# Optimization experiments

Hardware: AMD Instinct MI355X
Metric: run time of the kernel (lower is better)

Reference implementation:

```python
import jax, jax.numpy as jnp
import numpy as np

# ---- static config (matches init_kwargs) ----
D_MODEL = 2048
D_STATE = 64
D_CONV = 4
EXPAND = 2
HEADDIM = 64
NGROUPS = 1
CHUNK = 256
D_INNER = EXPAND * D_MODEL            # 4096
NHEADS = D_INNER // HEADDIM           # 64
CONV_DIM = D_INNER + 2 * NGROUPS * D_STATE   # 4224
D_IN_PROJ = 2 * D_INNER + 2 * NGROUPS * D_STATE + NHEADS  # 8384
EPS = 1e-5


def setup_inputs() -> dict:
    key = jax.random.key(0)
    ks = jax.random.split(key, 7)
    B, L = 2, 2048
    u = jax.random.normal(ks[0], (B, L, D_MODEL), jnp.float32)
    W_in = jax.random.normal(ks[1], (D_IN_PROJ, D_MODEL), jnp.float32) * (D_MODEL ** -0.5)
    conv_w = jax.random.normal(ks[2], (CONV_DIM, D_CONV), jnp.float32) * (D_CONV ** -0.5)
    conv_b = jnp.zeros((CONV_DIM,), jnp.float32)
    # dt_bias = softplus^{-1}(dt) with dt ~ LogUniform(1e-3, 1e-1), as in the torch init
    dt = jnp.exp(jax.random.uniform(ks[3], (NHEADS,), jnp.float32)
                 * (np.log(0.1) - np.log(0.001)) + np.log(0.001))
    dt_bias = dt + jnp.log(-jnp.expm1(-dt))
    A_log = jnp.log(jax.random.uniform(ks[4], (NHEADS,), jnp.float32, minval=1.0, maxval=16.0))
    D = jnp.ones((NHEADS,), jnp.float32)
    norm_w = jnp.ones((D_INNER,), jnp.float32)
    W_out = jax.random.normal(ks[5], (D_MODEL, D_INNER), jnp.float32) * (D_INNER ** -0.5)
    return dict(u=u, W_in=W_in, conv_w=conv_w, conv_b=conv_b, dt_bias=dt_bias,
                A_log=A_log, D=D, norm_w=norm_w, W_out=W_out)


def _chunked_ssd(x, dt, A, Bm, Cm):
    """Mamba2 chunked selective scan (ssd, discrete form).
    x:[b,l,h,p] dt:[b,l,h] A:[h] Bm,Cm:[b,l,n] (ngroups=1, broadcast over heads).
    Returns y:[b,l,h,p]."""
    b, l, h, p = x.shape
    c = l // CHUNK
    xc = x.reshape(b, c, CHUNK, h, p)
    dtc = dt.reshape(b, c, CHUNK, h)
    Bc = Bm.reshape(b, c, CHUNK, D_STATE)
    Cc = Cm.reshape(b, c, CHUNK, D_STATE)

    Abar = (dtc * A).transpose(0, 3, 1, 2)          # [b,h,c,s]
    Acum = jnp.cumsum(Abar, axis=-1)                # [b,h,c,s]

    # intra-chunk decay matrix L[i,j] = exp(sum_{k=j+1..i} Abar_k), lower-tri
    seg = Acum[..., :, None] - Acum[..., None, :]   # [b,h,c,s,s]
    tri = jnp.tril(jnp.ones((CHUNK, CHUNK), bool))
    Lmat = jnp.where(tri, jnp.exp(seg), 0.0)

    xdt = xc * dtc[..., None]                       # [b,c,s,h,p] (dt*B*x discretization)
    Y_diag = jnp.einsum('bcln,bcsn,bhcls,bcshp->bclhp', Cc, Bc, Lmat, xdt)

    # per-chunk final states
    decay_states = jnp.exp(Acum[..., -1:] - Acum)   # [b,h,c,s]
    states = jnp.einsum('bcsn,bhcs,bcshp->bchpn', Bc, decay_states, xdt)

    # inter-chunk recurrence (associative scan across chunk summaries)
    Achunk = Acum[..., -1]                          # [b,h,c]
    Acs = jnp.cumsum(jnp.pad(Achunk, ((0, 0), (0, 0), (1, 0))), axis=-1)  # [b,h,c+1]
    segc = Acs[..., :, None] - Acs[..., None, :]
    tric = jnp.tril(jnp.ones((c + 1, c + 1), bool))
    decay_chunk = jnp.where(tric, jnp.exp(segc), 0.0)          # [b,h,c+1,c+1]
    states0 = jnp.pad(states, ((0, 0), (1, 0), (0, 0), (0, 0), (0, 0)))  # zero init state
    new_states = jnp.einsum('bhzc,bchpn->bzhpn', decay_chunk, states0)
    prev_states = new_states[:, :-1]                # state entering each chunk [b,c,h,p,n]

    state_decay = jnp.exp(Acum)                     # [b,h,c,s]
    Y_off = jnp.einsum('bcln,bchpn,bhcl->bclhp', Cc, prev_states, state_decay)
    return (Y_diag + Y_off).reshape(b, l, h, p)


def reference(u, W_in, conv_w, conv_b, dt_bias, A_log, D, norm_w, W_out):
    b, l, _ = u.shape
    zxbcdt = u @ W_in.T                                        # [b,l,8384]
    z = zxbcdt[..., :D_INNER]
    xBC = zxbcdt[..., D_INNER:D_INNER + CONV_DIM]
    dt = jax.nn.softplus(zxbcdt[..., D_INNER + CONV_DIM:] + dt_bias)  # [b,l,h]

    # causal depthwise conv1d + SiLU
    xp = jnp.pad(xBC, ((0, 0), (D_CONV - 1, 0), (0, 0)))
    xBC = conv_b + sum(xp[:, w:w + l, :] * conv_w[:, w] for w in range(D_CONV))
    xBC = jax.nn.silu(xBC)

    x = xBC[..., :D_INNER].reshape(b, l, NHEADS, HEADDIM)
    Bm = xBC[..., D_INNER:D_INNER + D_STATE]
    Cm = xBC[..., D_INNER + D_STATE:]

    A = -jnp.exp(A_log)                                        # [h]
    y = _chunked_ssd(x, dt, A, Bm, Cm)                         # [b,l,h,p]
    y = y + x * D[None, None, :, None]                         # D skip on raw x
    y = y.reshape(b, l, D_INNER)

    # gated RMSNorm (norm_before_gate=False): gate first, then normalize
    y = y * jax.nn.silu(z)
    y = y * jax.lax.rsqrt(jnp.mean(y * y, axis=-1, keepdims=True) + EPS) * norm_w
    return y @ W_out.T
```

## Files before the change

### kernel.cpp

```cpp
#include <hip/hip_runtime.h>
#include <hip/hip_bf16.h>
#include <cstdint>

#define DPROJ  8384

typedef __attribute__((ext_vector_type(8))) short short8;
typedef __attribute__((ext_vector_type(4))) short sh4;
typedef __attribute__((ext_vector_type(2))) short sh2;
typedef __attribute__((ext_vector_type(4))) float f32x4;

#define ZX16_OFF   0ul
#define DTB_OFF    17170432ul
#define ACU_OFF    17432576ul
#define CBT_OFF    17694720ul
#define ST_OFF     18219008ul
#define YB_OFF     22413312ul
#define HALO_OFF   39190528ul
#define U16_OFF    39393280ul
#define WIN16_OFF  43587584ul
#define WOUT16_OFF 52172800ul

__device__ __forceinline__ short f2bf(float x) {
  union { float f; uint32_t u; } v{x};
  uint32_t r = (v.u + 0x7fff + ((v.u >> 16) & 1)) >> 16;
  return (short)r;
}
__device__ __forceinline__ float bf2f(short s) {
  union { uint32_t u; float f; } v;
  v.u = ((uint32_t)(uint16_t)s) << 16;
  return v.f;
}

__global__ __launch_bounds__(256) void cast3_bf16_kernel(
    const float* __restrict__ ina, short* __restrict__ outa, int n8a,
    const float* __restrict__ inb, short* __restrict__ outb, int n8b,
    const float* __restrict__ inc, short* __restrict__ outc, int n8c) {
  int i = blockIdx.x * 256 + threadIdx.x;
  const float* in;
  short* out;
  if (i < n8a) {
    in = ina; out = outa;
  } else if (i < n8a + n8b) {
    i -= n8a;
    in = inb; out = outb;
  } else {
    i -= n8a + n8b;
    if (i >= n8c) return;
    in = inc; out = outc;
  }
  const float4* p = (const float4*)(in + (size_t)i * 8);
  float4 a = p[0], b = p[1];
  short8 o;
  o[0] = f2bf(a.x); o[1] = f2bf(a.y); o[2] = f2bf(a.z); o[3] = f2bf(a.w);
  o[4] = f2bf(b.x); o[5] = f2bf(b.y); o[6] = f2bf(b.z); o[7] = f2bf(b.w);
  *(short8*)(out + (size_t)i * 8) = o;
}

__device__ __forceinline__ void gload16(const void* g, const void* l) {
  __builtin_amdgcn_global_load_lds(
      (const __attribute__((address_space(1))) void*)g,
      (__attribute__((address_space(3))) void*)l, 16, 0, 0);
}

template <int OUTBF>
__global__ __launch_bounds__(512) void gemm_big(
    const short* __restrict__ A, int lda, const short* __restrict__ B, int ldb,
    void* __restrict__ Cv, int ldc, int K, int Nvalid) {
  const int orig = blockIdx.x + gridDim.x * blockIdx.y;
  const int xcd = orig & 7;
  const int cid = orig >> 3;
  const int rpx = gridDim.y >> 3;
  const int tn = cid / rpx;
  const int tm = xcd * rpx + (cid % rpx);
  __shared__ __align__(16) short As[256 * 64];
  __shared__ __align__(16) short Bs[128 * 64];
  const int t = threadIdx.x;
  const int w = t >> 6, lane = t & 63;
  const int m0 = tm * 256, n0 = tn * 128;
  const int wr = (w >> 1) * 64, wc = (w & 1) * 64;
  const int fr = lane & 15;
  const int cik = lane >> 4;
  const int frs = fr & 7;
  const int rl = t >> 3;
  const int sch = ((t & 7) ^ (rl & 7)) << 3;
  const short* pa_[4];
  const short* pb_[2];
#pragma unroll
  for (int c = 0; c < 4; ++c)
    pa_[c] = A + (size_t)(m0 + c * 64 + rl) * lda + sch;
#pragma unroll
  for (int c = 0; c < 2; ++c) {
    int br = n0 + c * 64 + rl;
    if (br > Nvalid - 1) br = Nvalid - 1;
    pb_[c] = B + (size_t)br * ldb + sch;
  }
  f32x4 acc[4][4];
#pragma unroll
  for (int i = 0; i < 4; ++i)
#pragma unroll
    for (int j = 0; j < 4; ++j) acc[i][j] = (f32x4){0.f, 0.f, 0.f, 0.f};

  for (int k0 = 0; k0 < K; k0 += 64) {
#pragma unroll
    for (int c = 0; c < 4; ++c)
      gload16(pa_[c] + k0, &As[c * 4096 + w * 512 + lane * 8]);
#pragma unroll
    for (int c = 0; c < 2; ++c)
      gload16(pb_[c] + k0, &Bs[c * 4096 + w * 512 + lane * 8]);
    __syncthreads();
#pragma unroll
    for (int kk = 0; kk < 2; ++kk) {
      const int ci = kk * 4 + cik;
      short8 af[4], bg[4];
#pragma unroll
      for (int i = 0; i < 4; ++i) {
        const int ra = wr + i * 16 + fr;
        const int rb = wc + i * 16 + fr;
        af[i] = *(const short8*)&As[ra * 64 + ((ci ^ frs) << 3)];
        bg[i] = *(const short8*)&Bs[rb * 64 + ((ci ^ frs) << 3)];
      }
#pragma unroll
      for (int i = 0; i < 4; ++i)
#pragma unroll
        for (int j = 0; j < 4; ++j)
          acc[i][j] = __builtin_amdgcn_mfma_f32_16x16x32_bf16(af[i], bg[j],
                                                              acc[i][j], 0, 0, 0);
    }
    __syncthreads();
  }
#pragma unroll
  for (int i = 0; i < 4; ++i) {
    const int row = m0 + wr + i * 16 + (lane >> 4) * 4;
#pragma unroll
    for (int j = 0; j < 4; ++j) {
      const int col = n0 + wc + j * 16 + fr;
      if (col < Nvalid) {
#pragma unroll
        for (int r = 0; r < 4; ++r) {
          if (OUTBF)
            ((short*)Cv)[(size_t)(row + r) * ldc + col] = f2bf(acc[i][j][r]);
          else
            ((float*)Cv)[(size_t)(row + r) * ldc + col] = acc[i][j][r];
        }
      }
    }
  }
}

template <int OUTBF>
__global__ __launch_bounds__(256) void gemm_bf16(
    const short* __restrict__ A, int lda, const short* __restrict__ B, int ldb,
    void* __restrict__ Cv, int ldc, int K, int Nvalid) {
  const int orig = blockIdx.x + gridDim.x * blockIdx.y;
  const int xcd = orig & 7;
  const int cid = orig >> 3;
  const int rpx = gridDim.y >> 3;
  const int tn = cid / rpx;
  const int tm = xcd * rpx + (cid % rpx);
  __shared__ __align__(16) short As[128 * 64];
  __shared__ __align__(16) short Bs[128 * 64];
  const int t = threadIdx.x;
  const int w = t >> 6, lane = t & 63;
  const int m0 = tm * 128, n0 = tn * 128;
  const int wr = (w >> 1) * 64, wc = (w & 1) * 64;
  const int fr = lane & 15;
  const int cik = lane >> 4;
  const int frs = fr & 7;
  const int rl = lane >> 3;
  const int sch = ((lane & 7) ^ rl) << 3;
  const short* pa_[4];
  const short* pb_[4];
#pragma unroll
  for (int c = 0; c < 4; ++c) {
    int r = c * 32 + w * 8 + rl;
    pa_[c] = A + (size_t)(m0 + r) * lda + sch;
    int br = n0 + r;
    if (br > Nvalid - 1) br = Nvalid - 1;
    pb_[c] = B + (size_t)br * ldb + sch;
  }
  f32x4 acc[4][4];
#pragma unroll
  for (int i = 0; i < 4; ++i)
#pragma unroll
    for (int j = 0; j < 4; ++j) acc[i][j] = (f32x4){0.f, 0.f, 0.f, 0.f};

  for (int k0 = 0; k0 < K; k0 += 64) {
#pragma unroll
    for (int c = 0; c < 4; ++c) {
      gload16(pa_[c] + k0, &As[c * 2048 + w * 512 + lane * 8]);
      gload16(pb_[c] + k0, &Bs[c * 2048 + w * 512 + lane * 8]);
    }
    __syncthreads();
#pragma unroll
    for (int kk = 0; kk < 2; ++kk) {
      const int ci = kk * 4 + cik;
      short8 af[4], bg[4];
#pragma unroll
      for (int i = 0; i < 4; ++i) {
        const int ra = wr + i * 16 + fr;
        const int rb = wc + i * 16 + fr;
        af[i] = *(const short8*)&As[ra * 64 + ((ci ^ frs) << 3)];
        bg[i] = *(const short8*)&Bs[rb * 64 + ((ci ^ frs) << 3)];
      }
#pragma unroll
      for (int i = 0; i < 4; ++i)
#pragma unroll
        for (int j = 0; j < 4; ++j)
          acc[i][j] = __builtin_amdgcn_mfma_f32_16x16x32_bf16(af[i], bg[j],
                                                              acc[i][j], 0, 0, 0);
    }
    __syncthreads();
  }
#pragma unroll
  for (int i = 0; i < 4; ++i) {
    const int row = m0 + wr + i * 16 + (lane >> 4) * 4;
#pragma unroll
    for (int j = 0; j < 4; ++j) {
      const int col = n0 + wc + j * 16 + fr;
      if (col < Nvalid) {
#pragma unroll
        for (int r = 0; r < 4; ++r) {
          if (OUTBF)
            ((short*)Cv)[(size_t)(row + r) * ldc + col] = f2bf(acc[i][j][r]);
          else
            ((float*)Cv)[(size_t)(row + r) * ldc + col] = acc[i][j][r];
        }
      }
    }
  }
}

__global__ __launch_bounds__(256) void halo_dt_kernel(
    const short* __restrict__ zx, short* __restrict__ halo,
    const float* __restrict__ dt_bias, const float* __restrict__ A_log,
    float* __restrict__ dtb, float* __restrict__ acu) {
  __shared__ float sc[256];
  if (blockIdx.x < 1584) {
    int idx = blockIdx.x * 256 + threadIdx.x;
    int ch = idx % 4224;
    int r = idx / 4224;
    int j = r % 3;
    int r2 = r / 3;
    int lc = r2 & 15, b = r2 >> 4;
    int l = lc * 128 - 3 + j;
    halo[idx] =
        (l < 0) ? (short)0 : zx[(size_t)(b * 2048 + l) * DPROJ + 4096 + ch];
    return;
  }
  int bid = blockIdx.x - 1584;
  int c = bid & 7, h = (bid >> 3) & 63, b = bid >> 9;
  int s = threadIdx.x;
  int tok = b * 2048 + c * 256 + s;
  float raw = bf2f(zx[(size_t)tok * DPROJ + 8320 + h]) + dt_bias[h];
  float dtv = (raw > 20.f) ? raw : log1pf(expf(raw));
  float A = -expf(A_log[h]);
  sc[s] = dtv * A;
  __syncthreads();
  for (int off = 1; off < 256; off <<= 1) {
    float v = (s >= off) ? sc[s - off] : 0.f;
    __syncthreads();
    sc[s] += v;
    __syncthreads();
  }
  int o = (b * 64 + h) * 2048 + c * 256 + s;
  dtb[o] = dtv;
  acu[o] = sc[s];
}

__global__ __launch_bounds__(256) void conv_kernel(short* __restrict__ zx,
                                                   const short* __restrict__ halo,
                                                   const float* __restrict__ cw,
                                                   const float* __restrict__ cb) {
  int idx = blockIdx.x * 256 + threadIdx.x;
  int chp = idx % 2112;
  int r = idx / 2112;
  int ch = chp * 2;
  int lc = r & 15, b = r >> 4;
  float w0a = cw[ch * 4 + 0], w1a = cw[ch * 4 + 1], w2a = cw[ch * 4 + 2],
        w3a = cw[ch * 4 + 3];
  float w0b = cw[ch * 4 + 4], w1b = cw[ch * 4 + 5], w2b = cw[ch * 4 + 6],
        w3b = cw[ch * 4 + 7];
  float ba = cb[ch], bb = cb[ch + 1];
  const short* hp = halo + (size_t)r * 3 * 4224 + ch;
  sh2 h0 = *(const sh2*)hp;
  sh2 h1 = *(const sh2*)(hp + 4224);
  sh2 h2 = *(const sh2*)(hp + 8448);
  float xa3 = bf2f(h0[0]), xb3 = bf2f(h0[1]);
  float xa2 = bf2f(h1[0]), xb2 = bf2f(h1[1]);
  float xa1 = bf2f(h2[0]), xb1 = bf2f(h2[1]);
  size_t base = (size_t)(b * 2048 + lc * 128) * DPROJ + 4096 + ch;
  for (int i = 0; i < 128; ++i) {
    sh2 xv = *(const sh2*)&zx[base];
    float xa0 = bf2f(xv[0]), xb0 = bf2f(xv[1]);
    float va = ba + w0a * xa3 + w1a * xa2 + w2a * xa1 + w3a * xa0;
    float vb = bb + w0b * xb3 + w1b * xb2 + w2b * xb1 + w3b * xb0;
    va = va / (1.f + __expf(-va));
    vb = vb / (1.f + __expf(-vb));
    sh2 o;
    o[0] = f2bf(va);
    o[1] = f2bf(vb);
    *(sh2*)&zx[base] = o;
    xa3 = xa2; xa2 = xa1; xa1 = xa0;
    xb3 = xb2; xb2 = xb1; xb1 = xb0;
    base += DPROJ;
  }
}

__global__ __launch_bounds__(256) void cbt_states_kernel(
    const short* __restrict__ zx, const float* __restrict__ dtb,
    const float* __restrict__ acu, short* __restrict__ cbtT,
    float* __restrict__ st) {
  __shared__ __align__(16) char smem[35840];
  int t = threadIdx.x;
  if (blockIdx.x < 256) {
    float(*cl)[33] = (float(*)[33])smem;
    float(*blds)[32] = (float(*)[32])(smem + 33792);
    int bid = blockIdx.x;
    int sb = bid & 15, c = (bid >> 4) & 7, b = bid >> 7;
    int tok0 = b * 2048 + c * 256;
    float acc[16];
#pragma unroll
    for (int i = 0; i < 16; ++i) acc[i] = 0.f;
    for (int nh = 0; nh < 2; ++nh) {
      __syncthreads();
      for (int it = 0; it < 32; ++it) {
        int e = it * 256 + t;
        int row = e >> 5, n = e & 31;
        cl[row][n] =
            bf2f(zx[(size_t)(tok0 + row) * DPROJ + 8256 + nh * 32 + n]);
      }
      for (int it = 0; it < 2; ++it) {
        int e = it * 256 + t;
        int row = e >> 5, n = e & 31;
        blds[row][n] = bf2f(
            zx[(size_t)(tok0 + sb * 16 + row) * DPROJ + 8192 + nh * 32 + n]);
      }
      __syncthreads();
      for (int n = 0; n < 32; ++n) {
        float cv = cl[t][n];
#pragma unroll
        for (int s2 = 0; s2 < 16; ++s2) acc[s2] += cv * blds[s2][n];
      }
    }
    short* outp = cbtT + ((size_t)(b * 8 + c) * 256 + t) * 256 + sb * 16;
#pragma unroll
    for (int s2 = 0; s2 < 16; ++s2) outp[s2] = f2bf(acc[s2]);
    return;
  }
  short(*As2)[136] = (short(*)[136])smem;
  short(*Bs2)[136] = (short(*)[136])(smem + 17408);
  float* wl = (float*)(smem + 34816);
  int bid = blockIdx.x - 256;
  int h = bid & 63, c = (bid >> 6) & 7, b = bid >> 9;
  int w = t >> 6, lane = t & 63;
  int tok0 = b * 2048 + c * 256;
  int bh = (b * 64 + h) * 2048 + c * 256;
  {
    float aend = acu[bh + 255];
    wl[t] = __expf(aend - acu[bh + t]) * dtb[bh + t];
  }
  __syncthreads();
  const short* xbase = zx + (size_t)tok0 * DPROJ + 4096 + h * 64;
  const short* bbase = zx + (size_t)tok0 * DPROJ + 8192;
  const int fr = lane & 15, fko = (lane >> 4) * 8;
  const int wi = (w >> 1) * 32, wj = (w & 1) * 32;
  f32x4 acc2[2][2];
#pragma unroll
  for (int i = 0; i < 2; ++i)
#pragma unroll
    for (int j = 0; j < 2; ++j) acc2[i][j] = (f32x4){0.f, 0.f, 0.f, 0.f};

  for (int ph = 0; ph < 2; ++ph) {
    const int kb = ph * 128;
    if (ph) __syncthreads();
    for (int it = 0; it < 8; ++it) {
      int idx = it * 256 + t;
      int p = idx & 63, kg = idx >> 6;
      int k = kb + kg * 4;
      const short* xp = xbase + (size_t)k * DPROJ + p;
      const short* bp = bbase + (size_t)k * DPROJ + p;
      sh4 oa, ob;
#pragma unroll
      for (int r = 0; r < 4; ++r) {
        oa[r] = xp[(size_t)r * DPROJ];
        ob[r] = f2bf(bf2f(bp[(size_t)r * DPROJ]) * wl[k + r]);
      }
      *(sh4*)&As2[p][kg * 4] = oa;
      *(sh4*)&Bs2[p][kg * 4] = ob;
    }
    __syncthreads();
#pragma unroll
    for (int kk0 = 0; kk0 < 128; kk0 += 32) {
      short8 af[2], bg[2];
#pragma unroll
      for (int i = 0; i < 2; ++i) {
        af[i] = *(const short8*)&As2[wi + i * 16 + fr][kk0 + fko];
        bg[i] = *(const short8*)&Bs2[wj + i * 16 + fr][kk0 + fko];
      }
#pragma unroll
      for (int i = 0; i < 2; ++i)
#pragma unroll
        for (int j = 0; j < 2; ++j)
          acc2[i][j] = __builtin_amdgcn_mfma_f32_16x16x32_bf16(
              af[i], bg[j], acc2[i][j], 0, 0, 0);
    }
  }
  float* outp = st + ((size_t)(b * 8 + c) * 64 + h) * 4096;
  const int rq = (lane >> 4) * 4;
#pragma unroll
  for (int i = 0; i < 2; ++i) {
    int p0 = wi + i * 16 + rq;
#pragma unroll
    for (int j = 0; j < 2; ++j) {
      int n = wj + j * 16 + fr;
#pragma unroll
      for (int r = 0; r < 4; ++r)
        outp[(size_t)(p0 + r) * 64 + n] = acc2[i][j][r];
    }
  }
}

__global__ __launch_bounds__(256) void chunkscan_kernel(
    const float* __restrict__ acu, float* __restrict__ st) {
  int bid = blockIdx.x;
  int pc = bid & 15, h = (bid >> 4) & 63, b = bid >> 10;
  int pn = pc * 256 + threadIdx.x;
  int abase = (b * 64 + h) * 2048;
  float run = 0.f;
  for (int c = 0; c < 8; ++c) {
    size_t idx = ((size_t)(b * 8 + c) * 64 + h) * 4096 + pn;
    float s = st[idx];
    st[idx] = run;
    float ach = acu[abase + c * 256 + 255];
    run = run * __expf(ach) + s;
  }
}

__global__ __launch_bounds__(256) void ydiag_mfma(
    const short* __restrict__ zx, const float* __restrict__ dtb,
    const float* __restrict__ acu, const short* __restrict__ cbtT,
    const float* __restrict__ st, const float* __restrict__ Dp,
    short* __restrict__ yb) {
  __shared__ __align__(16) short Xs[64][328];
  __shared__ float acs[256];
  __shared__ float dts[256];
  int bid = blockIdx.x;
  int h = bid & 63, c = (bid >> 6) & 7, b = bid >> 9;
  int t = threadIdx.x;
  int w = t >> 6, lane = t & 63;
  int tok0 = b * 2048 + c * 256;
  int bh = (b * 64 + h) * 2048 + c * 256;
  acs[t] = acu[bh + t];
  dts[t] = dtb[bh + t];
  const short* xbase = zx + (size_t)tok0 * DPROJ + 4096 + h * 64;
  const float* st_b = st + ((size_t)(b * 8 + c) * 64 + h) * 4096;
  for (int it = 0; it < 16; ++it) {
    int idx = it * 256 + t;
    int p = idx & 63, kg = idx >> 6;
    const short* xp = xbase + (size_t)(kg * 4) * DPROJ + p;
    sh4 o;
    o[0] = xp[0];
    o[1] = xp[DPROJ];
    o[2] = xp[2 * DPROJ];
    o[3] = xp[3 * DPROJ];
    *(sh4*)&Xs[p][kg * 4] = o;
  }
  for (int it = 0; it < 4; ++it) {
    int idx = it * 256 + t;
    int ng = idx & 15, p = idx >> 4;
    float4 v = *(const float4*)&st_b[p * 64 + ng * 4];
    sh4 o;
    o[0] = f2bf(v.x); o[1] = f2bf(v.y); o[2] = f2bf(v.z); o[3] = f2bf(v.w);
    *(sh4*)&Xs[p][256 + ng * 4] = o;
  }
  __syncthreads();

  const int fr = lane & 15, fko = (lane >> 4) * 8;
  float Al[4], eAl[4];
#pragma unroll
  for (int i = 0; i < 4; ++i) {
    Al[i] = acs[(i * 4 + w) * 16 + fr];
    eAl[i] = __expf(Al[i]);
  }
  f32x4 acc[4][4];
#pragma unroll
  for (int i = 0; i < 4; ++i)
#pragma unroll
    for (int j = 0; j < 4; ++j) acc[i][j] = (f32x4){0.f, 0.f, 0.f, 0.f};

  const short* cbt_b = cbtT + (size_t)(b * 8 + c) * 65536;

  const int k0max = (12 + w) * 16 + 16;
  for (int k0 = 0; k0 < k0max; k0 += 32) {
    short8 bg[4];
#pragma unroll
    for (int j = 0; j < 4; ++j)
      bg[j] = *(const short8*)&Xs[j * 16 + fr][k0 + fko];
    const int bi = (k0 + 32 < 256) ? (k0 + 32) : 255;
    const float base = acs[bi];
    float vd[8];
#pragma unroll
    for (int jj = 0; jj < 8; ++jj) {
      int s = k0 + fko + jj;
      vd[jj] = __expf(base - acs[s]) * dts[s];
    }
#pragma unroll
    for (int i = 0; i < 4; ++i) {
      const int li0 = (i * 4 + w) * 16;
      if (k0 > li0 + 15) continue;
      const int l = li0 + fr;
      const short8 cb = *(const short8*)&cbt_b[(size_t)l * 256 + k0 + fko];
      short8 af;
      if (k0 + 32 <= li0) {
        const float u = __expf(Al[i] - base);
#pragma unroll
        for (int jj = 0; jj < 8; ++jj)
          af[jj] = f2bf(bf2f(cb[jj]) * (vd[jj] * u));
      } else {
#pragma unroll
        for (int jj = 0; jj < 8; ++jj) {
          int s = k0 + fko + jj;
          float wv = 0.f;
          if (s <= l) wv = bf2f(cb[jj]) * __expf(Al[i] - acs[s]) * dts[s];
          af[jj] = f2bf(wv);
        }
      }
#pragma unroll
      for (int j = 0; j < 4; ++j)
        acc[i][j] = __builtin_amdgcn_mfma_f32_16x16x32_bf16(af, bg[j],
                                                            acc[i][j], 0, 0, 0);
    }
  }
#pragma unroll
  for (int k0 = 256; k0 < 320; k0 += 32) {
    short8 bg[4];
#pragma unroll
    for (int j = 0; j < 4; ++j)
      bg[j] = *(const short8*)&Xs[j * 16 + fr][k0 + fko];
#pragma unroll
    for (int i = 0; i < 4; ++i) {
      const int l = (i * 4 + w) * 16 + fr;
      const short8 cv = *(const short8*)(zx + (size_t)(tok0 + l) * DPROJ +
                                         8256 + (k0 - 256) + fko);
      short8 af;
#pragma unroll
      for (int jj = 0; jj < 8; ++jj) af[jj] = f2bf(bf2f(cv[jj]) * eAl[i]);
#pragma unroll
      for (int j = 0; j < 4; ++j)
        acc[i][j] = __builtin_amdgcn_mfma_f32_16x16x32_bf16(af, bg[j],
                                                            acc[i][j], 0, 0, 0);
    }
  }
  float Dh = Dp[h];
  const int rq = (lane >> 4) * 4;
#pragma unroll
  for (int i = 0; i < 4; ++i) {
    int l0 = (i * 4 + w) * 16 + rq;
#pragma unroll
    for (int j = 0; j < 4; ++j) {
      int p = j * 16 + fr;
      sh4 x4 = *(const sh4*)&Xs[p][l0];
      f32x4 a = acc[i][j];
#pragma unroll
      for (int r = 0; r < 4; ++r)
        yb[(size_t)(bh + l0 + r) * 64 + p] = f2bf(a[r] + Dh * bf2f(x4[r]));
    }
  }
}

__global__ __launch_bounds__(256) void gatenorm_kernel(
    short* zx, const float* __restrict__ nw, const short* __restrict__ yb) {
  int tok = blockIdx.x;
  int b = tok >> 11, l = tok & 2047;
  int t = threadIdx.x;
  const int d0 = t * 16;
  const int h = d0 >> 6, p0 = d0 & 63;
  short8 yv8[2], zv8[2];
  yv8[0] = *(const short8*)&yb[((size_t)(b * 64 + h) * 2048 + l) * 64 + p0];
  yv8[1] = *(const short8*)&yb[((size_t)(b * 64 + h) * 2048 + l) * 64 + p0 + 8];
  zv8[0] = *(const short8*)&zx[(size_t)tok * DPROJ + d0];
  zv8[1] = *(const short8*)&zx[(size_t)tok * DPROJ + d0 + 8];
  float g[16];
  float ss = 0.f;
#pragma unroll
  for (int i = 0; i < 16; ++i) {
    float yv = bf2f(yv8[i >> 3][i & 7]);
    float zv = bf2f(zv8[i >> 3][i & 7]);
    float gv = yv * (zv / (1.f + __expf(-zv)));
    g[i] = gv;
    ss += gv * gv;
  }
  for (int off = 32; off > 0; off >>= 1) ss += __shfl_down(ss, off);
  __shared__ float red[4];
  int wid = t >> 6, lane = t & 63;
  if (lane == 0) red[wid] = ss;
  __syncthreads();
  float tot = red[0] + red[1] + red[2] + red[3];
  float scale = rsqrtf(tot * (1.f / 4096.f) + 1e-5f);
  short8 o[2];
#pragma unroll
  for (int i = 0; i < 16; ++i)
    o[i >> 3][i & 7] = f2bf(g[i] * scale * nw[d0 + i]);
  *(short8*)&zx[(size_t)tok * DPROJ + d0] = o[0];
  *(short8*)&zx[(size_t)tok * DPROJ + d0 + 8] = o[1];
}

extern "C" void kernel_launch(void* const* d_in, const int* in_sizes, int n_in,
                              void* d_out, int out_size, void* d_ws,
                              size_t ws_size, hipStream_t stream) {
  const float* u = (const float*)d_in[0];
  const float* W_in = (const float*)d_in[1];
  const float* conv_w = (const float*)d_in[2];
  const float* conv_b = (const float*)d_in[3];
  const float* dt_bias = (const float*)d_in[4];
  const float* A_log = (const float*)d_in[5];
  const float* Dp = (const float*)d_in[6];
  const float* norm_w = (const float*)d_in[7];
  const float* W_out = (const float*)d_in[8];
  float* out = (float*)d_out;
  float* ws = (float*)d_ws;

  short* zx16 = (short*)(ws + ZX16_OFF);
  float* dtb = ws + DTB_OFF;
  float* acu = ws + ACU_OFF;
  short* cbtT = (short*)(ws + CBT_OFF);
  float* st = ws + ST_OFF;
  short* yb = (short*)(ws + YB_OFF);
  short* halo = (short*)(ws + HALO_OFF);
  short* u16 = (short*)(ws + U16_OFF);
  short* win16 = (short*)(ws + WIN16_OFF);
  short* wout16 = (short*)(ws + WOUT16_OFF);

  cast3_bf16_kernel<<<16576, 256, 0, stream>>>(u, u16, 1048576, W_in, win16,
                                               2146304, W_out, wout16, 1048576);
  gemm_big<1><<<dim3(66, 16), 512, 0, stream>>>(u16, 2048, win16, 2048, zx16,
                                                DPROJ, 2048, DPROJ);
  halo_dt_kernel<<<2608, 256, 0, stream>>>(zx16, halo, dt_bias, A_log, dtb,
                                           acu);
  conv_kernel<<<264, 256, 0, stream>>>(zx16, halo, conv_w, conv_b);
  cbt_states_kernel<<<1280, 256, 0, stream>>>(zx16, dtb, acu, cbtT, st);
  chunkscan_kernel<<<2048, 256, 0, stream>>>(acu, st);
  ydiag_mfma<<<1024, 256, 0, stream>>>(zx16, dtb, acu, cbtT, st, Dp, yb);
  gatenorm_kernel<<<4096, 256, 0, stream>>>(zx16, norm_w, yb);
  gemm_bf16<0><<<dim3(16, 32), 256, 0, stream>>>(zx16, DPROJ, wout16, 4096, out,
                                                 2048, 4096, 2048);
}
```

Baseline: 435.4 us.

## Double-buffer gemm_big LDS tiles with K-step 32 and prefetch next tile

Splits the GEMM K loop into 32-wide steps and keeps two LDS buffers for A and B. The next tile is issued via global_load_lds before computing on the current one, so there is one barrier per iteration instead of two. The swizzle changes to a 4-chunk XOR pattern to suit 32-wide rows. Each barrier now covers only half as much MFMA work, and with no explicit vmcnt wait the prefetch may not actually be complete when the next iteration reads it.

```diff
diff --git a/kernel.cpp b/kernel.cpp
--- a/kernel.cpp
+++ b/kernel.cpp
@@ -72,62 +72,60 @@
   const int rpx = gridDim.y >> 3;
   const int tn = cid / rpx;
   const int tm = xcd * rpx + (cid % rpx);
-  __shared__ __align__(16) short As[256 * 64];
-  __shared__ __align__(16) short Bs[128 * 64];
+  __shared__ __align__(16) short As[2][256 * 32];
+  __shared__ __align__(16) short Bs[2][128 * 32];
   const int t = threadIdx.x;
   const int w = t >> 6, lane = t & 63;
   const int m0 = tm * 256, n0 = tn * 128;
   const int wr = (w >> 1) * 64, wc = (w & 1) * 64;
   const int fr = lane & 15;
-  const int cik = lane >> 4;
-  const int frs = fr & 7;
-  const int rl = t >> 3;
-  const int sch = ((t & 7) ^ (rl & 7)) << 3;
-  const short* pa_[4];
-  const short* pb_[2];
-#pragma unroll
-  for (int c = 0; c < 4; ++c)
-    pa_[c] = A + (size_t)(m0 + c * 64 + rl) * lda + sch;
-#pragma unroll
-  for (int c = 0; c < 2; ++c) {
-    int br = n0 + c * 64 + rl;
-    if (br > Nvalid - 1) br = Nvalid - 1;
-    pb_[c] = B + (size_t)br * ldb + sch;
-  }
+  const int ci = lane >> 4;
+  const int srow = t >> 2;
+  const int sch = (((t & 3) ^ (srow & 3)) << 3);
+  const short* pa0 = A + (size_t)(m0 + srow) * lda + sch;
+  const short* pa1 = A + (size_t)(m0 + 128 + srow) * lda + sch;
+  int br = n0 + srow;
+  if (br > Nvalid - 1) br = Nvalid - 1;
+  const short* pb0 = B + (size_t)br * ldb + sch;
   f32x4 acc[4][4];
 #pragma unroll
   for (int i = 0; i < 4; ++i)
 #pragma unroll
     for (int j = 0; j < 4; ++j) acc[i][j] = (f32x4){0.f, 0.f, 0.f, 0.f};
 
-  for (int k0 = 0; k0 < K; k0 += 64) {
-#pragma unroll
-    for (int c = 0; c < 4; ++c)
-      gload16(pa_[c] + k0, &As[c * 4096 + w * 512 + lane * 8]);
-#pragma unroll
-    for (int c = 0; c < 2; ++c)
-      gload16(pb_[c] + k0, &Bs[c * 4096 + w * 512 + lane * 8]);
+  const int nt = K >> 5;
+
+#define STAGE(kt, bb)                                                          \
+  {                                                                            \
+    const int ko_ = (kt) << 5;                                                 \
+    gload16(pa0 + ko_, &As[bb][t * 8]);                                        \
+    gload16(pa1 + ko_, &As[bb][4096 + t * 8]);                                 \
+    gload16(pb0 + ko_, &Bs[bb][t * 8]);                                        \
+  }
+
+  STAGE(0, 0);
+  __syncthreads();
+  for (int kt = 0; kt < nt; ++kt) {
+    if (kt + 1 < nt) STAGE(kt + 1, (kt + 1) & 1);
+    const int cb = kt & 1;
+    short8 af[4], bg[4];
+#pragma unroll
+    for (int i = 0; i < 4; ++i) {
+      const int ra = wr + i * 16 + fr;
+      const int rb = wc + i * 16 + fr;
+      af[i] = *(const short8*)&As[cb][ra * 32 + ((ci ^ (ra & 3)) << 3)];
+      bg[i] = *(const short8*)&Bs[cb][rb * 32 + ((ci ^ (rb & 3)) << 3)];
+    }
+#pragma unroll
+    for (int i = 0; i < 4; ++i)
+#pragma unroll
+      for (int j = 0; j < 4; ++j)
+        acc[i][j] = __builtin_amdgcn_mfma_f32_16x16x32_bf16(af[i], bg[j],
+                                                            acc[i][j], 0, 0, 0);
     __syncthreads();
-#pragma unroll
-    for (int kk = 0; kk < 2; ++kk) {
-      const int ci = kk * 4 + cik;
-      short8 af[4], bg[4];
-#pragma unroll
-      for (int i = 0; i < 4; ++i) {
-        const int ra = wr + i * 16 + fr;
-        const int rb = wc + i * 16 + fr;
-        af[i] = *(const short8*)&As[ra * 64 + ((ci ^ frs) << 3)];
-        bg[i] = *(const short8*)&Bs[rb * 64 + ((ci ^ frs) << 3)];
-      }
-#pragma unroll
-      for (int i = 0; i < 4; ++i)
-#pragma unroll
-        for (int j = 0; j < 4; ++j)
-          acc[i][j] = __builtin_amdgcn_mfma_f32_16x16x32_bf16(af[i], bg[j],
-                                                              acc[i][j], 0, 0, 0);
-    }
-    __syncthreads();
-  }
+  }
+#undef STAGE
+
 #pragma unroll
   for (int i = 0; i < 4; ++i) {
     const int row = m0 + wr + i * 16 + (lane >> 4) * 4;
```

Measured after the change: 452.3 us. +3.9%, slower.
